# Optimization experiments

Measured on AMD Instinct MI355X. Metric: run time of the kernel, lower is better.

Reference implementation:

```python
import jax, jax.numpy as jnp
import numpy as np

N_BINS = 15


def setup_inputs() -> dict:
    key = jax.random.key(0)
    k1, k2 = jax.random.split(key)
    N, C = 2_000_000, 100
    logits = jax.random.normal(k1, (N, C), dtype=jnp.float32)
    labels = jax.random.randint(k2, (N,), 0, C, dtype=jnp.int64)
    return {"logits": logits, "labels": labels}


def reference(logits, labels):
    # softmax confidences + predictions
    probs = jax.nn.softmax(logits, axis=1)
    conf = jnp.max(probs, axis=1)            # [N]
    pred = jnp.argmax(probs, axis=1)          # [N]
    acc = (pred == labels).astype(conf.dtype)  # [N]

    # torch loop uses bins (lower, upper] with boundaries linspace(0,1,16).
    # conf in ((b-1)/B, b/B] maps to bin b-1 == ceil(conf*B)-1 (clipped).
    bin_idx = jnp.clip(jnp.ceil(conf * N_BINS).astype(jnp.int32) - 1, 0, N_BINS - 1)

    counts = jax.ops.segment_sum(jnp.ones_like(conf), bin_idx, num_segments=N_BINS)
    sum_conf = jax.ops.segment_sum(conf, bin_idx, num_segments=N_BINS)
    sum_acc = jax.ops.segment_sum(acc, bin_idx, num_segments=N_BINS)

    nonempty = counts > 0
    safe = jnp.where(nonempty, counts, jnp.ones_like(counts))
    gap = jnp.abs(sum_conf / safe - sum_acc / safe)  # |avg_conf - acc| per bin

    n_total = jnp.asarray(conf.shape[0], conf.dtype)
    ece = jnp.sum(jnp.where(nonempty, gap * counts / n_total, 0.0))
    mce = jnp.max(jnp.where(nonempty, gap, -jnp.inf))
    mce = jnp.where(jnp.any(nonempty), mce, jnp.asarray(1.0, conf.dtype))
    return ece, mce
```

## Files before the change

### kernel.cpp

```cpp
#include <hip/hip_runtime.h>
#include <math.h>

#define NBINS 15

template<int CTRL>
__device__ __forceinline__ float dpp_f(float x) {
    return __int_as_float(__builtin_amdgcn_update_dpp(
        0, __float_as_int(x), CTRL, 0xF, 0xF, true));
}
template<int CTRL>
__device__ __forceinline__ int dpp_i(int x) {
    return __builtin_amdgcn_update_dpp(0, x, CTRL, 0xF, 0xF, true);
}
#define QP_XOR1 0xB1
#define QP_XOR2 0x4E

__global__ __launch_bounds__(256) void ce_rows100(const float* __restrict__ logits,
                                                  const int* __restrict__ labels,
                                                  float* __restrict__ gbins, int N) {
    __shared__ float sb[NBINS * 3];
    if (threadIdx.x < NBINS * 3) sb[threadIdx.x] = 0.f;
    __syncthreads();

    const int lane = threadIdx.x & 63;
    const int q = lane & 3;
    const int rq = lane >> 2;
    const int gw = (blockIdx.x * blockDim.x + threadIdx.x) >> 6;
    const int nw = (gridDim.x * blockDim.x) >> 6;
    const int nchunks = (N + 15) >> 4;

    for (int chunk = gw; chunk < nchunks; chunk += nw) {
        const int row = chunk * 16 + rq;
        if (row < N) {
            const float* rpf = logits + (size_t)row * 100;
            const float4* rp = reinterpret_cast<const float4*>(rpf);
            const int lab = labels[row];

            float m = -INFINITY, s = 0.f;
            int arg = 0;
            #pragma unroll
            for (int k = 0; k < 6; ++k) {
                const int qi = 4 * k + q;
                float4 v = rp[qi];
                const int bi = qi * 4;
                { float x = v.x; if (x > m) { s *= __expf(m - x); m = x; arg = bi;     } s += __expf(x - m); }
                { float x = v.y; if (x > m) { s *= __expf(m - x); m = x; arg = bi + 1; } s += __expf(x - m); }
                { float x = v.z; if (x > m) { s *= __expf(m - x); m = x; arg = bi + 2; } s += __expf(x - m); }
                { float x = v.w; if (x > m) { s *= __expf(m - x); m = x; arg = bi + 3; } s += __expf(x - m); }
            }
            {
                float x = rpf[96 + q];
                if (x > m) { s *= __expf(m - x); m = x; arg = 96 + q; }
                s += __expf(x - m);
            }

            const float ml = m;
            float M = m; int A = arg;
            {
                float t = dpp_f<QP_XOR1>(M); int ti = dpp_i<QP_XOR1>(A);
                if (t > M || (t == M && ti < A)) { M = t; A = ti; }
                t = dpp_f<QP_XOR2>(M); ti = dpp_i<QP_XOR2>(A);
                if (t > M || (t == M && ti < A)) { M = t; A = ti; }
            }
            float sc = s * __expf(ml - M);
            sc += dpp_f<QP_XOR1>(sc);
            sc += dpp_f<QP_XOR2>(sc);

            if (q == 0) {
                const float conf = 1.0f / sc;
                int b = (int)ceilf(conf * (float)NBINS) - 1;
                b = min(max(b, 0), NBINS - 1);
                atomicAdd(&sb[b * 3 + 0], 1.0f);
                atomicAdd(&sb[b * 3 + 1], conf);
                if (A == lab) atomicAdd(&sb[b * 3 + 2], 1.0f);
            }
        }
    }

    __syncthreads();
    if (threadIdx.x < NBINS * 3) {
        float v = sb[threadIdx.x];
        if (v != 0.f) atomicAdd(&gbins[threadIdx.x], v);
    }
}

__global__ __launch_bounds__(256) void ce_rows_generic(const float* __restrict__ logits,
                                                       const int* __restrict__ labels,
                                                       float* __restrict__ gbins,
                                                       int N, int C) {
    __shared__ float sb[NBINS * 3];
    if (threadIdx.x < NBINS * 3) sb[threadIdx.x] = 0.f;
    __syncthreads();

    const int r = blockIdx.x * blockDim.x + threadIdx.x;
    if (r < N) {
        const float* rp = logits + (size_t)r * (size_t)C;
        float m = -INFINITY, s = 0.f;
        int arg = 0;
        for (int k = 0; k < C; ++k) {
            float x = rp[k];
            if (x > m) { s *= __expf(m - x); m = x; arg = k; }
            s += __expf(x - m);
        }
        float conf = 1.0f / s;
        int b = (int)ceilf(conf * (float)NBINS) - 1;
        b = min(max(b, 0), NBINS - 1);
        atomicAdd(&sb[b * 3 + 0], 1.0f);
        atomicAdd(&sb[b * 3 + 1], conf);
        if (arg == labels[r]) atomicAdd(&sb[b * 3 + 2], 1.0f);
    }
    __syncthreads();
    if (threadIdx.x < NBINS * 3) {
        float v = sb[threadIdx.x];
        if (v != 0.f) atomicAdd(&gbins[threadIdx.x], v);
    }
}

__global__ void ce_final(const float* __restrict__ gbins, float* __restrict__ out,
                         float inv_n) {
    int t = threadIdx.x;
    float gap = 0.f, w = 0.f;
    bool ne = false;
    if (t < NBINS) {
        float c = gbins[t * 3 + 0];
        float sc = gbins[t * 3 + 1];
        float sa = gbins[t * 3 + 2];
        if (c > 0.f) { ne = true; gap = fabsf(sc / c - sa / c); w = c; }
    }
    float ece = ne ? gap * w * inv_n : 0.f;
    float mce = ne ? gap : -INFINITY;
    #pragma unroll
    for (int off = 1; off < 64; off <<= 1) {
        ece += __shfl_xor(ece, off);
        mce = fmaxf(mce, __shfl_xor(mce, off));
    }
    if (t == 0) {
        out[0] = ece;
        out[1] = (mce == -INFINITY) ? 1.0f : mce;
    }
}

extern "C" void kernel_launch(void* const* d_in, const int* in_sizes, int n_in,
                              void* d_out, int out_size, void* d_ws, size_t ws_size,
                              hipStream_t stream) {
    const float* logits = (const float*)d_in[0];
    const int* labels = (const int*)d_in[1];
    int N = in_sizes[1];
    int C = in_sizes[0] / in_sizes[1];

    float* gbins = (float*)d_ws;
    (void)hipMemsetAsync(gbins, 0, NBINS * 3 * sizeof(float), stream);

    if (C == 100) {
        ce_rows100<<<2048, 256, 0, stream>>>(logits, labels, gbins, N);
    } else {
        ce_rows_generic<<<(N + 255) / 256, 256, 0, stream>>>(logits, labels, gbins, N, C);
    }
    ce_final<<<1, 64, 0, stream>>>(gbins, (float*)d_out, 1.0f / (float)N);
}
```

Before: 155.5 us.

## Software-pipeline row loads and fuse final reduction via last-block ticket

Each wave now prefetches the next chunk's logits and label into registers while it computes softmax and argmax on the current chunk, so memory latency can overlap with the exp math. The separate finalization kernel is removed: a global ticket counter lets the last block to finish compute ECE and MCE, which saves one kernel launch. The cost is higher register pressure from the double-buffered float4s, plus a threadfence and atomic per block.

```diff
diff --git a/kernel.cpp b/kernel.cpp
--- a/kernel.cpp
+++ b/kernel.cpp
@@ -17,9 +17,15 @@
 
 __global__ __launch_bounds__(256) void ce_rows100(const float* __restrict__ logits,
                                                   const int* __restrict__ labels,
-                                                  float* __restrict__ gbins, int N) {
+                                                  float* __restrict__ gbins,
+                                                  unsigned int* __restrict__ ticket,
+                                                  float* __restrict__ out,
+                                                  int N, float inv_n,
+                                                  unsigned int nblocks) {
     __shared__ float sb[NBINS * 3];
+    __shared__ int slast;
     if (threadIdx.x < NBINS * 3) sb[threadIdx.x] = 0.f;
+    if (threadIdx.x == 0) slast = 0;
     __syncthreads();
 
     const int lane = threadIdx.x & 63;
@@ -29,31 +35,70 @@
     const int nw = (gridDim.x * blockDim.x) >> 6;
     const int nchunks = (N + 15) >> 4;
 
-    for (int chunk = gw; chunk < nchunks; chunk += nw) {
+    float4 c0, c1, c2, c3, c4, c5;
+    float ct = 0.f;
+    int clab = 0;
+    int chunk = gw;
+    {
         const int row = chunk * 16 + rq;
-        if (row < N) {
+        if (chunk < nchunks && row < N) {
             const float* rpf = logits + (size_t)row * 100;
             const float4* rp = reinterpret_cast<const float4*>(rpf);
-            const int lab = labels[row];
-
-            float m = -INFINITY, s = 0.f;
-            int arg = 0;
-            #pragma unroll
-            for (int k = 0; k < 6; ++k) {
-                const int qi = 4 * k + q;
-                float4 v = rp[qi];
-                const int bi = qi * 4;
-                { float x = v.x; if (x > m) { s *= __expf(m - x); m = x; arg = bi;     } s += __expf(x - m); }
-                { float x = v.y; if (x > m) { s *= __expf(m - x); m = x; arg = bi + 1; } s += __expf(x - m); }
-                { float x = v.z; if (x > m) { s *= __expf(m - x); m = x; arg = bi + 2; } s += __expf(x - m); }
-                { float x = v.w; if (x > m) { s *= __expf(m - x); m = x; arg = bi + 3; } s += __expf(x - m); }
-            }
-            {
-                float x = rpf[96 + q];
-                if (x > m) { s *= __expf(m - x); m = x; arg = 96 + q; }
-                s += __expf(x - m);
-            }
-
+            clab = labels[row];
+            c0 = rp[q];      c1 = rp[4 + q];  c2 = rp[8 + q];
+            c3 = rp[12 + q]; c4 = rp[16 + q]; c5 = rp[20 + q];
+            ct = rpf[96 + q];
+        }
+    }
+
+    while (chunk < nchunks) {
+        const int row = chunk * 16 + rq;
+        const bool rv = row < N;
+        const int nchunk_i = chunk + nw;
+        const int nrow = nchunk_i * 16 + rq;
+        const bool nv = (nchunk_i < nchunks) && (nrow < N);
+        const float* nrpf = logits + (size_t)nrow * 100;
+        const float4* nrp = reinterpret_cast<const float4*>(nrpf);
+
+        float4 n0, n1, n2, n3, n4, n5;
+        float nt = 0.f;
+        int nlab = 0;
+        const int lab = clab;
+
+        float m = -INFINITY, s = 0.f;
+        int arg = 0;
+        auto cons = [&](const float4& v, int bi) {
+            { float x = v.x; if (x > m) { s *= __expf(m - x); m = x; arg = bi;     } s += __expf(x - m); }
+            { float x = v.y; if (x > m) { s *= __expf(m - x); m = x; arg = bi + 1; } s += __expf(x - m); }
+            { float x = v.z; if (x > m) { s *= __expf(m - x); m = x; arg = bi + 2; } s += __expf(x - m); }
+            { float x = v.w; if (x > m) { s *= __expf(m - x); m = x; arg = bi + 3; } s += __expf(x - m); }
+        };
+
+        if (rv & nv) {
+            nlab = labels[nrow];
+            cons(c0, 4 * q);       n0 = nrp[q];
+            cons(c1, 16 + 4 * q);  n1 = nrp[4 + q];
+            cons(c2, 32 + 4 * q);  n2 = nrp[8 + q];
+            cons(c3, 48 + 4 * q);  n3 = nrp[12 + q];
+            cons(c4, 64 + 4 * q);  n4 = nrp[16 + q];
+            cons(c5, 80 + 4 * q);  n5 = nrp[20 + q];
+            { float x = ct; if (x > m) { s *= __expf(m - x); m = x; arg = 96 + q; } s += __expf(x - m); }
+            nt = nrpf[96 + q];
+        } else {
+            if (rv) {
+                cons(c0, 4 * q);      cons(c1, 16 + 4 * q); cons(c2, 32 + 4 * q);
+                cons(c3, 48 + 4 * q); cons(c4, 64 + 4 * q); cons(c5, 80 + 4 * q);
+                { float x = ct; if (x > m) { s *= __expf(m - x); m = x; arg = 96 + q; } s += __expf(x - m); }
+            }
+            if (nv) {
+                nlab = labels[nrow];
+                n0 = nrp[q];      n1 = nrp[4 + q];  n2 = nrp[8 + q];
+                n3 = nrp[12 + q]; n4 = nrp[16 + q]; n5 = nrp[20 + q];
+                nt = nrpf[96 + q];
+            }
+        }
+
+        if (rv) {
             const float ml = m;
             float M = m; int A = arg;
             {
@@ -75,12 +120,46 @@
                 if (A == lab) atomicAdd(&sb[b * 3 + 2], 1.0f);
             }
         }
+
+        c0 = n0; c1 = n1; c2 = n2; c3 = n3; c4 = n4; c5 = n5;
+        ct = nt; clab = nlab;
+        chunk = nchunk_i;
     }
 
     __syncthreads();
     if (threadIdx.x < NBINS * 3) {
         float v = sb[threadIdx.x];
         if (v != 0.f) atomicAdd(&gbins[threadIdx.x], v);
+    }
+    __syncthreads();
+    if (threadIdx.x == 0) {
+        __threadfence();
+        unsigned int t = atomicAdd(ticket, 1u);
+        if (t == nblocks - 1) slast = 1;
+    }
+    __syncthreads();
+    if (slast && threadIdx.x < 64) {
+        __threadfence();
+        int t = threadIdx.x;
+        float gap = 0.f, w = 0.f;
+        bool ne = false;
+        if (t < NBINS) {
+            float c  = atomicAdd(&gbins[t * 3 + 0], 0.f);
+            float sc = atomicAdd(&gbins[t * 3 + 1], 0.f);
+            float sa = atomicAdd(&gbins[t * 3 + 2], 0.f);
+            if (c > 0.f) { ne = true; gap = fabsf(sc / c - sa / c); w = c; }
+        }
+        float ece = ne ? gap * w * inv_n : 0.f;
+        float mce = ne ? gap : -INFINITY;
+        #pragma unroll
+        for (int off = 1; off < 64; off <<= 1) {
+            ece += __shfl_xor(ece, off);
+            mce = fmaxf(mce, __shfl_xor(mce, off));
+        }
+        if (t == 0) {
+            out[0] = ece;
+            out[1] = (mce == -INFINITY) ? 1.0f : mce;
+        }
     }
 }
 
@@ -149,12 +228,17 @@
     int C = in_sizes[0] / in_sizes[1];
 
     float* gbins = (float*)d_ws;
-    (void)hipMemsetAsync(gbins, 0, NBINS * 3 * sizeof(float), stream);
+    unsigned int* ticket = (unsigned int*)(gbins + NBINS * 3);
 
     if (C == 100) {
-        ce_rows100<<<2048, 256, 0, stream>>>(logits, labels, gbins, N);
+        (void)hipMemsetAsync(gbins, 0, (NBINS * 3 + 1) * sizeof(float), stream);
+        const unsigned int nblocks = 2048;
+        ce_rows100<<<nblocks, 256, 0, stream>>>(logits, labels, gbins, ticket,
+                                                (float*)d_out, N, 1.0f / (float)N,
+                                                nblocks);
     } else {
+        (void)hipMemsetAsync(gbins, 0, NBINS * 3 * sizeof(float), stream);
         ce_rows_generic<<<(N + 255) / 256, 256, 0, stream>>>(logits, labels, gbins, N, C);
-    }
-    ce_final<<<1, 64, 0, stream>>>(gbins, (float*)d_out, 1.0f / (float)N);
-}
+        ce_final<<<1, 64, 0, stream>>>(gbins, (float*)d_out, 1.0f / (float)N);
+    }
+}
```

Result: slower. 247.4 us (+59.1%).
